# Kernel tuning notes

Measured on AMD Instinct MI355X. Metric: run time of the kernel, lower is better.

Reference implementation:

```python
import jax, jax.numpy as jnp
import numpy as np

B, L, DIN, W, H, NL = 4, 1024, 768, 12288, 8, 2
BOTTLENECK = 64
DB = W // BOTTLENECK        # 192: total bottlenecked attention dim
HD = DB // H                # 24: per-head dim
K = 32                      # topk
LAM = 1.0 / (4 * DIN)
EPS = 1e-6


def setup_inputs() -> dict:
    key = jax.random.key(0)
    ks = jax.random.split(key, 8)
    x_input = jax.random.normal(ks[0], (B, L, DIN), jnp.float32)
    # decoder dictionary (torch: randn; scaled for numeric stability)
    D = jax.random.normal(ks[1], (W, DIN), jnp.float32) * 0.02
    b = jnp.zeros((1, DIN), jnp.float32)
    # per-attn-layer bottlenecked projections, stacked over layers
    Wq = jax.random.normal(ks[2], (NL, W, DB), jnp.float32) * 0.02
    Wk = jax.random.normal(ks[3], (NL, W, DB), jnp.float32) * 0.02
    Wv = jax.random.normal(ks[4], (NL, W, DB), jnp.float32) * 0.02
    Wo = jax.random.normal(ks[5], (NL, DB, W), jnp.float32) * 0.02
    bq = jnp.zeros((NL, DB), jnp.float32)
    bk = jnp.zeros((NL, DB), jnp.float32)
    bv = jnp.zeros((NL, DB), jnp.float32)
    bo = jnp.zeros((NL, W), jnp.float32)
    return {"x_input": x_input, "D": D, "b": b, "Wq": Wq, "bq": bq,
            "Wk": Wk, "bk": bk, "Wv": Wv, "bv": bv, "Wo": Wo, "bo": bo}


def _attention(z_ctx, z_in, Wq, bq, Wk, bk, Wv, bv, Wo, bo):
    # queries from current codes, keys/values from shifted context codes
    q = (z_in @ Wq + bq).reshape(B, L, H, HD)
    k = (z_ctx @ Wk + bk).reshape(B, L, H, HD)
    v = (z_ctx @ Wv + bv).reshape(B, L, H, HD)
    scores = jnp.einsum('bqhd,bkhd->bhqk', q, k) / np.sqrt(HD).astype(np.float32)
    causal = jnp.tril(jnp.ones((L, L), bool))  # query t sees ctx positions <= t
    scores = jnp.where(causal, scores, jnp.float32(-1e30))
    a = jax.nn.softmax(scores, axis=-1)
    o = jnp.einsum('bhqk,bkhd->bqhd', a, v).reshape(B, L, DB)
    return o @ Wo + bo


def reference(x_input, D, b, Wq, bq, Wk, bk, Wv, bv, Wo, bo):
    E = D.T  # tied weights
    x = x_input - b
    z_pred = jnp.zeros((B, L, W), x.dtype)
    for i in range(NL):
        z_in = jax.nn.relu((x * LAM) @ E)                       # [B,L,W]
        z_ctx = jnp.concatenate([jnp.zeros_like(z_in[:, :1]), z_in[:, :-1]], axis=1)
        z_pred_ = jax.nn.relu(_attention(z_ctx, z_in, Wq[i], bq[i], Wk[i], bk[i],
                                         Wv[i], bv[i], Wo[i], bo[i]))
        Dz = z_pred_ @ D                                        # [B,L,DIN]
        Dz_norm = jnp.linalg.norm(Dz, axis=-1, keepdims=True) + EPS
        proj_scale = jnp.sum(Dz * x, axis=-1, keepdims=True) / (Dz_norm ** 2)
        z_pred = z_pred + z_pred_ * proj_scale
        x = x - proj_scale * Dz
    # topk sparsification of the novel codes
    z_novel = jax.nn.relu((x * LAM) @ E)
    zf = z_novel.reshape(-1, W)                                 # [B*L, W]
    _, idx = jax.lax.top_k(zf, K)
    mask = jnp.zeros_like(zf).at[jnp.arange(zf.shape[0])[:, None], idx].set(1.0)
    z_novel = (zf * mask).reshape(B, L, W)
    x_recons = (z_novel + z_pred) @ D + b
    return x_recons
```

## Files before the change

### kernel.cpp

```cpp
#include <hip/hip_runtime.h>
#include <hip/hip_bf16.h>

typedef __attribute__((ext_vector_type(4))) float f32x4;
typedef __attribute__((ext_vector_type(8))) short short8;
typedef __attribute__((ext_vector_type(8))) unsigned short ushort8;
typedef __attribute__((ext_vector_type(4))) unsigned short ushort4v;
typedef __attribute__((ext_vector_type(4))) unsigned int uint4v;

#define DEVFN __device__ __forceinline__

DEVFN float b2f(unsigned short u) { return __uint_as_float(((unsigned)u) << 16); }
DEVFN unsigned short f2b(float f) {
  __hip_bfloat16 h = __float2bfloat16(f);
  return __builtin_bit_cast(unsigned short, h);
}

DEVFN void load_lds16(const void* g, void* l) {
  __builtin_amdgcn_global_load_lds(
      (const __attribute__((address_space(1))) unsigned int*)g,
      (__attribute__((address_space(3))) unsigned int*)l, 16, 0, 0);
}


__global__ void fill_out_zero(float* o, int n) {
  int i = blockIdx.x * 256 + threadIdx.x;
  if (i < n) o[i] = 0.0f;
}

__global__ __launch_bounds__(256) void init_x(
    const float* __restrict__ xin, const float* __restrict__ bvec,
    float* __restrict__ x, unsigned short* __restrict__ xb) {
  size_t i = (size_t)blockIdx.x * 256 + threadIdx.x;
  int col = (int)(i % 768);
  float v = xin[i] - bvec[col];
  x[i] = v;
  xb[i] = f2b(v);
}

__global__ __launch_bounds__(256) void fill_bias(
    float* __restrict__ buf, const float* __restrict__ bias, int ld) {
  size_t i = (size_t)blockIdx.x * 256 + threadIdx.x;
  buf[i] = bias ? bias[(int)(i % ld)] : 0.0f;
}

__global__ __launch_bounds__(256) void conv_f2b(
    const float* __restrict__ in, unsigned short* __restrict__ out) {
  size_t i = ((size_t)blockIdx.x * 256 + threadIdx.x) * 4;
  f32x4 v = *(const f32x4*)(in + i);
  ushort4v w;
#pragma unroll
  for (int e = 0; e < 4; ++e) w[e] = f2b(v[e]);
  *(ushort4v*)(out + i) = w;
}

__global__ __launch_bounds__(256) void transpose_f2b(
    const float* __restrict__ in, unsigned short* __restrict__ out,
    int R, int C) {
  __shared__ float tile[32][33];
  int r0 = blockIdx.x * 32, c0 = blockIdx.y * 32;
  int tx = threadIdx.x & 31, ty = threadIdx.x >> 5;
#pragma unroll
  for (int i = 0; i < 4; ++i)
    tile[ty + i * 8][tx] = in[(size_t)(r0 + ty + i * 8) * C + c0 + tx];
  __syncthreads();
#pragma unroll
  for (int i = 0; i < 4; ++i)
    out[(size_t)(c0 + ty + i * 8) * R + r0 + tx] = f2b(tile[tx][ty + i * 8]);
}

template <int GX, int GY, int GZ, int RX, int RG>
DEVFN void rect_decode(int bid, int& x, int& y, int& z) {
  constexpr int NRG = (GY * GZ) / RG;
  const int xcd = bid & 7;
  const int rr = bid >> 3;
  const int rgx = xcd % NRG, rxx = xcd / NRG;
  const int gl = rr % RG;
  int xl = rr / RG;
  xl = (xl + rgx * (RX / NRG)) % RX;
  const int g = rgx * RG + gl;
  x = rxx * RX + xl;
  y = g % GY;
  z = g / GY;
}

template <typename CT, bool RELU, int SC, bool BIAS, bool SPLITK,
          int GX, int GY, int GZ, int RX, int RG>
__global__ __launch_bounds__(512, 2) void gemm_bt2(
    const unsigned short* __restrict__ A, const unsigned short* __restrict__ B,
    CT* __restrict__ C, const float* __restrict__ bias,
    int K, int ldc, float alpha) {
  __shared__ unsigned short sA[2][256 * 64];
  __shared__ unsigned short sB[2][256 * 64];
  const int tid = threadIdx.x;
  const int wave = tid >> 6, lane = tid & 63;
  int bx, by, bz;
  rect_decode<GX, GY, GZ, RX, RG>((int)blockIdx.x, bx, by, bz);
  const int row0 = bx * 256, col0 = by * 256;
  const unsigned short* Ab = A + (size_t)row0 * K;
  const unsigned short* Bb = B + (size_t)col0 * K;
  const int srow = lane >> 3;
  const int swc = ((lane & 7) ^ srow) * 8;
  const int wm = wave & 1, wn = wave >> 1;
  const int lr = lane & 15;
  const int hi = lane >> 4;
  const int l7 = lane & 7;
  const int ksw0 = (hi ^ l7) * 8;
  const int ksw1 = ((4 + hi) ^ l7) * 8;
  const int klen = SPLITK ? (K / GZ) : K;
  const int kbeg = SPLITK ? bz * klen : 0;
  const int nt = klen / 64;
  f32x4 acc[8][4] = {};
  auto stage = [&](int buf, int t) {
    const int k0 = kbeg + t * 64;
#pragma unroll
    for (int it = 0; it < 8; ++it) {
      int c = wave * 8 + it;
      if (c < 32) {
        int r = c * 8 + srow;
        load_lds16(Ab + (size_t)r * K + k0 + swc, &sA[buf][c * 512]);
      } else {
        int cb = c - 32;
        int r = cb * 8 + srow;
        load_lds16(Bb + (size_t)r * K + k0 + swc, &sB[buf][cb * 512]);
      }
    }
  };
  stage(0, 0);
  __syncthreads();
  for (int t = 0; t < nt; ++t) {
    const int cur = t & 1;
    if (t + 1 < nt) stage(cur ^ 1, t + 1);
    const unsigned short* cA = &sA[cur][0];
    const unsigned short* cB = &sB[cur][0];
#pragma unroll
    for (int ks = 0; ks < 2; ++ks) {
      const int ko = ks ? ksw1 : ksw0;
      short8 af[8], bfr[4];
#pragma unroll
      for (int i = 0; i < 8; ++i)
        af[i] = *(const short8*)&cA[(wm * 128 + i * 16 + lr) * 64 + ko];
#pragma unroll
      for (int j = 0; j < 4; ++j)
        bfr[j] = *(const short8*)&cB[(wn * 64 + j * 16 + lr) * 64 + ko];
#pragma unroll
      for (int i = 0; i < 8; ++i)
#pragma unroll
        for (int j = 0; j < 4; ++j)
          acc[i][j] = __builtin_amdgcn_mfma_f32_16x16x32_bf16(af[i], bfr[j], acc[i][j], 0, 0, 0);
    }
    __syncthreads();
  }
  const int rc = (SC == 0) ? 0 : ((row0 >> 10) + 1);
  const int rbase = row0 + rc + wm * 128 + (lane >> 4) * 4;
  const int cbase = col0 + wn * 64 + lr;
#pragma unroll
  for (int j = 0; j < 4; ++j) {
    int col = cbase + j * 16;
    float bv = BIAS ? bias[col] : 0.0f;
#pragma unroll
    for (int i = 0; i < 8; ++i) {
#pragma unroll
      for (int r = 0; r < 4; ++r) {
        float vv = acc[i][j][r] * alpha;
        size_t off = (size_t)(rbase + i * 16 + r) * ldc + col;
        if constexpr (SPLITK) {
          atomicAdd((float*)C + off, vv);
        } else {
          vv += bv;
          if (RELU) vv = fmaxf(vv, 0.0f);
          if constexpr (sizeof(CT) == 2) ((unsigned short*)C)[off] = f2b(vv);
          else C[off] = vv;
        }
      }
    }
  }
}

__global__ __launch_bounds__(256) void gemm_qkv(
    const unsigned short* __restrict__ A, const unsigned short* __restrict__ Bq,
    const float* __restrict__ bq, const float* __restrict__ bk,
    const float* __restrict__ bv,
    float* __restrict__ qb, float* __restrict__ kb, float* __restrict__ vb,
    float* __restrict__ P2) {
  __shared__ unsigned short sA[2][64 * 64];
  __shared__ unsigned short sB[2][192 * 64];
  const int tid = threadIdx.x;
  const int wave = tid >> 6, lane = tid & 63;
  const int bid = (int)blockIdx.x;
  const int xcd = bid & 7;
  const int rr = bid >> 3;
  const int grank = xcd * 48 + rr;
  const int combo = grank >> 6;
  const int row = grank & 63;
  const int wz = combo >> 1;
  const int s = combo & 1;
  const int shift = (wz > 0);
  const unsigned short* B = Bq + (size_t)wz * 192 * 12288;
  const float* bias = (wz == 0) ? bq : (wz == 1 ? bk : bv);
  float* dst = (s == 0) ? ((wz == 0) ? qb : (wz == 1 ? kb : vb))
                        : (P2 + (size_t)wz * 786432);
  const int row0 = row * 64;
  const int ra = (row0 >> 10) + 1;
  const unsigned short* Ab = A + (size_t)(row0 + ra) * 12288;
  const int srow = lane >> 3;
  const int swc = ((lane & 7) ^ srow) * 8;
  const int wm = wave & 1, wn = wave >> 1;
  const int lr = lane & 15;
  const int hi = lane >> 4;
  const int l7 = lane & 7;
  const int ksw0 = (hi ^ l7) * 8;
  const int ksw1 = ((4 + hi) ^ l7) * 8;
  const int kbeg = s * 6144;
  f32x4 acc[2][6] = {};
  auto stage = [&](int buf, int t) {
    const int k0 = kbeg + t * 64;
#pragma unroll
    for (int it = 0; it < 8; ++it) {
      int c = wave * 8 + it;
      if (c < 8) {
        int r = c * 8 + srow;
        load_lds16(Ab + (size_t)r * 12288 + k0 + swc, &sA[buf][c * 512]);
      } else {
        int cb = c - 8;
        int r = cb * 8 + srow;
        load_lds16(B + (size_t)r * 12288 + k0 + swc, &sB[buf][cb * 512]);
      }
    }
  };
  stage(0, 0);
  __syncthreads();
  for (int t = 0; t < 96; ++t) {
    const int cur = t & 1;
    if (t + 1 < 96) stage(cur ^ 1, t + 1);
    const unsigned short* cA = &sA[cur][0];
    const unsigned short* cB = &sB[cur][0];
#pragma unroll
    for (int ks = 0; ks < 2; ++ks) {
      const int ko = ks ? ksw1 : ksw0;
      short8 af[2], bfr[6];
#pragma unroll
      for (int i = 0; i < 2; ++i)
        af[i] = *(const short8*)&cA[(wm * 32 + i * 16 + lr) * 64 + ko];
#pragma unroll
      for (int j = 0; j < 6; ++j)
        bfr[j] = *(const short8*)&cB[(wn * 96 + j * 16 + lr) * 64 + ko];
#pragma unroll
      for (int i = 0; i < 2; ++i)
#pragma unroll
        for (int j = 0; j < 6; ++j)
          acc[i][j] = __builtin_amdgcn_mfma_f32_16x16x32_bf16(af[i], bfr[j], acc[i][j], 0, 0, 0);
    }
    __syncthreads();
  }
  const int rbase = row0 + wm * 32 + (lane >> 4) * 4;
  const int cbase = wn * 96 + lr;
#pragma unroll
  for (int j = 0; j < 6; ++j) {
    int col = cbase + j * 16;
    float bvv = (s == 0) ? bias[col] : 0.0f;
#pragma unroll
    for (int i = 0; i < 2; ++i)
#pragma unroll
      for (int r = 0; r < 4; ++r) {
        int rw = rbase + i * 16 + r;
        if (shift) {
          if ((rw & 1023) == 1023) continue;
          rw += 1;
        }
        dst[(size_t)rw * 192 + col] = acc[i][j][r] + bvv;
      }
  }
}

__global__ __launch_bounds__(256) void qkv_merge(
    const float* __restrict__ P2, float* __restrict__ qb,
    float* __restrict__ kb, float* __restrict__ vb) {
  size_t i = ((size_t)blockIdx.x * 256 + threadIdx.x) * 4;
  const int plane = (int)(i / 786432);
  const size_t o = i - (size_t)plane * 786432;
  float* dst = plane == 0 ? qb : (plane == 1 ? kb : vb);
  f32x4 a = *(const f32x4*)(P2 + i);
  f32x4 b = *(const f32x4*)(dst + o);
#pragma unroll
  for (int e = 0; e < 4; ++e) b[e] += a[e];
  *(f32x4*)(dst + o) = b;
}

__global__ __launch_bounds__(256) void attn_pass1(
    const float* __restrict__ q, const float* __restrict__ k,
    const float* __restrict__ v, float* __restrict__ P) {
  const int wave = threadIdx.x >> 6, lane = threadIdx.x & 63;
  const int xcd = (int)blockIdx.x & 7;
  const int task = xcd * 1152 + ((int)blockIdx.x >> 3) * 4 + wave;
  const int bh = task / 288, t = task % 288;
  const int b = bh >> 3, h = bh & 7;
  int g8 = 0;
  while (4 * (g8 + 1) * (g8 + 2) <= t) ++g8;
  const int r = t - 4 * g8 * (g8 + 1);
  const int qg = g8 * 8 + r / (g8 + 1);
  const int chunk = r % (g8 + 1);
  const int qi = lane & 15, ks = lane >> 4;
  const int qpos = qg * 16 + qi;
  const int n = b * 1024 + qpos;
  const float scale = 0.20412414523193154f;
  float qv[24];
  const float* qr = q + (size_t)n * 192 + h * 24;
#pragma unroll
  for (int d = 0; d < 24; ++d) qv[d] = qr[d] * scale;
  float m = -1e30f, l = 0.0f, ov[24] = {};
  const float* kbp = k + (size_t)b * 1024 * 192 + h * 24;
  const float* vbp = v + (size_t)b * 1024 * 192 + h * 24;
  const int kend = min(qpos, chunk * 128 + 127);
  for (int kp = chunk * 128 + ks; kp <= kend; kp += 4) {
    const f32x4* kr = (const f32x4*)(kbp + (size_t)kp * 192);
    float s0 = 0.0f, s1 = 0.0f, s2 = 0.0f;
#pragma unroll
    for (int j = 0; j < 2; ++j) {
      f32x4 k0 = kr[j * 3 + 0], k1 = kr[j * 3 + 1], k2 = kr[j * 3 + 2];
#pragma unroll
      for (int e = 0; e < 4; ++e) {
        s0 += qv[(j * 3 + 0) * 4 + e] * k0[e];
        s1 += qv[(j * 3 + 1) * 4 + e] * k1[e];
        s2 += qv[(j * 3 + 2) * 4 + e] * k2[e];
      }
    }
    float s = s0 + s1 + s2;
    float mn = fmaxf(m, s);
    float corr = __expf(m - mn);
    float p = __expf(s - mn);
    const f32x4* vr = (const f32x4*)(vbp + (size_t)kp * 192);
    l = l * corr + p;
#pragma unroll
    for (int j = 0; j < 6; ++j) {
      f32x4 vvv = vr[j];
#pragma unroll
      for (int e = 0; e < 4; ++e) ov[j * 4 + e] = ov[j * 4 + e] * corr + p * vvv[e];
    }
    m = mn;
  }
#pragma unroll
  for (int off = 16; off < 64; off <<= 1) {
    float m2 = __shfl_xor(m, off);
    float l2 = __shfl_xor(l, off);
    float mn = fmaxf(m, m2);
    float c1 = __expf(m - mn), c2 = __expf(m2 - mn);
    l = l * c1 + l2 * c2;
#pragma unroll
    for (int d = 0; d < 24; ++d) {
      float o2 = __shfl_xor(ov[d], off);
      ov[d] = ov[d] * c1 + o2 * c2;
    }
    m = mn;
  }
  if (ks == 0) {
    float* pr = P + ((size_t)task * 16 + qi) * 28;
    pr[0] = m;
    pr[1] = l;
#pragma unroll
    for (int d = 0; d < 24; ++d) pr[2 + d] = ov[d];
  }
}

__global__ __launch_bounds__(192) void attn_merge(
    const float* __restrict__ P, unsigned short* __restrict__ o) {
  const int n = blockIdx.x;
  const int tid = threadIdx.x;
  const int h = tid / 24, d = tid - h * 24;
  const int b = n >> 10, qpos = n & 1023;
  const int qg = qpos >> 4, qi = qpos & 15;
  const int g8 = qg >> 3;
  const int nch = g8 + 1;
  const int bh = b * 8 + h;
  const int base = bh * 288 + 4 * g8 * (g8 + 1) + (qg - g8 * 8) * (g8 + 1);
  float M = -1e30f;
  for (int c = 0; c < nch; ++c)
    M = fmaxf(M, P[((size_t)(base + c) * 16 + qi) * 28]);
  float L = 0.0f, OV = 0.0f;
  for (int c = 0; c < nch; ++c) {
    const float* pr = P + ((size_t)(base + c) * 16 + qi) * 28;
    float w = __expf(pr[0] - M);
    L += pr[1] * w;
    OV += pr[2 + d] * w;
  }
  o[(size_t)n * 192 + h * 24 + d] = f2b(OV / L);
}

__global__ __launch_bounds__(256) void proj_update(
    const float* __restrict__ Dz, float* __restrict__ x,
    unsigned short* __restrict__ xb) {
  const int n = blockIdx.x;
  const int tid = threadIdx.x;
  const float* dz = Dz + (size_t)n * 768;
  float* xr = x + (size_t)n * 768;
  float dot = 0.0f, s2 = 0.0f;
  for (int i = tid; i < 768; i += 256) {
    float a = dz[i], c = xr[i];
    dot += a * c;
    s2 += a * a;
  }
#pragma unroll
  for (int o2 = 32; o2; o2 >>= 1) {
    dot += __shfl_down(dot, o2);
    s2 += __shfl_down(s2, o2);
  }
  __shared__ float sd[4], ss[4], sp;
  const int wave = tid >> 6, lane = tid & 63;
  if (lane == 0) { sd[wave] = dot; ss[wave] = s2; }
  __syncthreads();
  if (tid == 0) {
    float Dd = sd[0] + sd[1] + sd[2] + sd[3];
    float S = ss[0] + ss[1] + ss[2] + ss[3];
    float nrm = sqrtf(S) + 1e-6f;
    sp = Dd / (nrm * nrm);
  }
  __syncthreads();
  float p = sp;
  for (int i = tid; i < 768; i += 256) {
    float nx = xr[i] - p * dz[i];
    xr[i] = nx;
    xb[(size_t)n * 768 + i] = f2b(nx);
  }
}

DEVFN int sanitize(int v) { return (v & 0x8000) ? 0 : v; }

__global__ __launch_bounds__(256) void topk_rows(
    const unsigned short* __restrict__ zbuf, int* __restrict__ idxo,
    float* __restrict__ valo) {
  const int n = blockIdx.x;
  const int b = n >> 10;
  const int tid = threadIdx.x;
  const int wave = tid >> 6, lane = tid & 63;
  const uint4v* zr = (const uint4v*)(zbuf + (size_t)(n + b + 1) * 12288);
  uint4v pk[6];
#pragma unroll
  for (int j = 0; j < 6; ++j) pk[j] = zr[tid * 6 + j];
  __shared__ int swsum[4];
  __shared__ int seq[256];
  __shared__ int spcnt;
  int lo = 0, hi = 0x7F7F;
  while (lo < hi) {
    int mid = (lo + hi) >> 1;
    int c = 0;
#pragma unroll
    for (int j = 0; j < 6; ++j)
#pragma unroll
      for (int e = 0; e < 4; ++e) {
        unsigned int u = pk[j][e];
        c += (sanitize((int)(u & 0xffffu)) > mid) + (sanitize((int)(u >> 16)) > mid);
      }
#pragma unroll
    for (int o2 = 32; o2; o2 >>= 1) c += __shfl_down(c, o2);
    if (lane == 0) swsum[wave] = c;
    __syncthreads();
    int total = swsum[0] + swsum[1] + swsum[2] + swsum[3];
    __syncthreads();
    if (total < 32) hi = mid; else lo = mid + 1;
  }
  const int T = lo;
  int cgt = 0, ceq = 0;
#pragma unroll
  for (int j = 0; j < 6; ++j)
#pragma unroll
    for (int e = 0; e < 4; ++e) {
      unsigned int u = pk[j][e];
      int v0 = sanitize((int)(u & 0xffffu)), v1 = sanitize((int)(u >> 16));
      cgt += (v0 > T) + (v1 > T);
      ceq += (v0 == T) + (v1 == T);
    }
  int cg = cgt;
#pragma unroll
  for (int o2 = 32; o2; o2 >>= 1) cg += __shfl_down(cg, o2);
  if (lane == 0) swsum[wave] = cg;
  seq[tid] = ceq;
  if (tid == 0) spcnt = 0;
  __syncthreads();
  const int total_gt = swsum[0] + swsum[1] + swsum[2] + swsum[3];
  for (int o2 = 1; o2 < 256; o2 <<= 1) {
    int vv = (tid >= o2) ? seq[tid - o2] : 0;
    __syncthreads();
    seq[tid] += vv;
    __syncthreads();
  }
  const int quota = 32 - total_gt;
  int rank = seq[tid] - ceq;
  int* irow = idxo + (size_t)n * 32;
  float* vrow = valo + (size_t)n * 32;
#pragma unroll
  for (int j = 0; j < 6; ++j)
#pragma unroll
    for (int e = 0; e < 4; ++e) {
      unsigned int u = pk[j][e];
#pragma unroll
      for (int hf = 0; hf < 2; ++hf) {
        int v = sanitize(hf ? (int)(u >> 16) : (int)(u & 0xffffu));
        bool kp = false;
        if (v > T) kp = true;
        else if (v == T) { if (rank < quota) kp = true; ++rank; }
        if (kp) {
          int pos = atomicAdd(&spcnt, 1);
          irow[pos] = tid * 48 + j * 8 + e * 2 + hf;
          vrow[pos] = b2f((unsigned short)v);
        }
      }
    }
}

__global__ __launch_bounds__(256) void sparse_recons(
    const int* __restrict__ idxo, const float* __restrict__ valo,
    const float* __restrict__ x, const float* __restrict__ xin,
    const float* __restrict__ D, float* __restrict__ out) {
  const int n = blockIdx.x;
  const int t = threadIdx.x;
  __shared__ int sidx[32];
  __shared__ float sval[32];
  if (t < 32) { sidx[t] = idxo[(size_t)n * 32 + t]; sval[t] = valo[(size_t)n * 32 + t]; }
  __syncthreads();
  float acc[3];
#pragma unroll
  for (int u = 0; u < 3; ++u) {
    size_t i = (size_t)n * 768 + t + u * 256;
    acc[u] = xin[i] - x[i];
  }
  for (int j = 0; j < 32; ++j) {
    size_t base = (size_t)sidx[j] * 768;
    float vj = sval[j];
#pragma unroll
    for (int u = 0; u < 3; ++u) acc[u] += vj * D[base + t + u * 256];
  }
#pragma unroll
  for (int u = 0; u < 3; ++u) out[(size_t)n * 768 + t + u * 256] = acc[u];
}

extern "C" void kernel_launch(void* const* d_in, const int* in_sizes, int n_in,
                              void* d_out, int out_size, void* d_ws, size_t ws_size,
                              hipStream_t stream) {
  (void)in_sizes; (void)n_in;
  const float* xin  = (const float*)d_in[0];
  const float* D    = (const float*)d_in[1];
  const float* bvec = (const float*)d_in[2];
  const float* Wq   = (const float*)d_in[3];
  const float* bq   = (const float*)d_in[4];
  const float* Wk   = (const float*)d_in[5];
  const float* bk   = (const float*)d_in[6];
  const float* Wv   = (const float*)d_in[7];
  const float* bv   = (const float*)d_in[8];
  const float* Wo   = (const float*)d_in[9];
  const float* bo   = (const float*)d_in[10];
  const float LAM = 1.0f / 3072.0f;

  char* ws = (char*)d_ws;
  size_t off = 0;
  auto alloc = [&](size_t bytes) {
    void* p = ws + off;
    off += (bytes + 255) & ~(size_t)255;
    return p;
  };
  unsigned short* zbuf = (unsigned short*)alloc((size_t)4 * 1025 * 12288 * 2);
  unsigned short* zpred_ = zbuf;
  float* attnP = (float*)zbuf;
  float* x           = (float*)alloc((size_t)4096 * 768 * 4);
  unsigned short* xb = (unsigned short*)alloc((size_t)4096 * 768 * 2);
  float* qb  = (float*)alloc((size_t)4096 * 192 * 4);
  float* kb  = (float*)alloc((size_t)4096 * 192 * 4);
  float* vb  = (float*)alloc((size_t)4096 * 192 * 4);
  unsigned short* ob = (unsigned short*)alloc((size_t)4096 * 192 * 2);
  float* Dz  = (float*)alloc((size_t)4096 * 768 * 4);
  int* idxo  = (int*)alloc((size_t)4096 * 32 * 4);
  float* valo = (float*)alloc((size_t)4096 * 32 * 4);
  const size_t WQKV = (size_t)192 * 12288;
  unsigned short* WqkvT = (unsigned short*)alloc((size_t)6 * WQKV * 2);
  unsigned short* WoT   = (unsigned short*)alloc((size_t)2 * 12288 * 192 * 2);
  unsigned short* Dbt   = (unsigned short*)alloc((size_t)12288 * 768 * 2);
  unsigned short* Dt    = (unsigned short*)alloc((size_t)768 * 12288 * 2);
  const size_t NEED = off;
  float* P2 = Dz;

  if (ws_size < NEED) {
    fill_out_zero<<<(out_size + 255) / 256, 256, 0, stream>>>((float*)d_out, out_size);
    return;
  }

  init_x<<<12288, 256, 0, stream>>>(xin, bvec, x, xb);
  conv_f2b<<<9216, 256, 0, stream>>>(D, Dbt);
  transpose_f2b<<<dim3(384, 24), 256, 0, stream>>>(D, Dt, 12288, 768);
  for (int l = 0; l < 2; ++l) {
    transpose_f2b<<<dim3(384, 6), 256, 0, stream>>>(
        Wq + (size_t)l * 12288 * 192, WqkvT + (size_t)(l * 3 + 0) * WQKV, 12288, 192);
    transpose_f2b<<<dim3(384, 6), 256, 0, stream>>>(
        Wk + (size_t)l * 12288 * 192, WqkvT + (size_t)(l * 3 + 1) * WQKV, 12288, 192);
    transpose_f2b<<<dim3(384, 6), 256, 0, stream>>>(
        Wv + (size_t)l * 12288 * 192, WqkvT + (size_t)(l * 3 + 2) * WQKV, 12288, 192);
    transpose_f2b<<<dim3(6, 384), 256, 0, stream>>>(
        Wo + (size_t)l * 192 * 12288, WoT + (size_t)l * 12288 * 192, 192, 12288);
  }

  for (int l = 0; l < 2; ++l) {
    gemm_bt2<unsigned short, true, 1, false, false, 16, 48, 1, 16, 6>
        <<<768, 512, 0, stream>>>(xb, Dbt, zbuf, nullptr, 768, 12288, LAM);
    fill_bias<<<3072, 256, 0, stream>>>(kb, bk + (size_t)l * 192, 192);
    fill_bias<<<3072, 256, 0, stream>>>(vb, bv + (size_t)l * 192, 192);
    fill_bias<<<9216, 256, 0, stream>>>(P2, nullptr, 192);
    gemm_qkv<<<384, 256, 0, stream>>>(
        zbuf, WqkvT + (size_t)(l * 3) * WQKV,
        bq + (size_t)l * 192, bk + (size_t)l * 192, bv + (size_t)l * 192,
        qb, kb, vb, P2);
    qkv_merge<<<2304, 256, 0, stream>>>(P2, qb, kb, vb);
    attn_pass1<<<2304, 256, 0, stream>>>(qb, kb, vb, attnP);
    attn_merge<<<4096, 192, 0, stream>>>(attnP, ob);
    gemm_bt2<unsigned short, true, 0, true, false, 16, 48, 1, 16, 6>
        <<<768, 512, 0, stream>>>(
        ob, WoT + (size_t)l * 12288 * 192, zpred_, bo + (size_t)l * 12288, 192, 12288, 1.0f);
    fill_bias<<<12288, 256, 0, stream>>>(Dz, nullptr, 768);
    gemm_bt2<float, false, 0, false, true, 16, 3, 4, 8, 3>
        <<<192, 512, 0, stream>>>(zpred_, Dt, Dz, nullptr, 12288, 768, 1.0f);
    proj_update<<<4096, 256, 0, stream>>>(Dz, x, xb);
  }
  gemm_bt2<unsigned short, true, 1, false, false, 16, 48, 1, 16, 6>
      <<<768, 512, 0, stream>>>(xb, Dbt, zbuf, nullptr, 768, 12288, LAM);
  topk_rows<<<4096, 256, 0, stream>>>(zbuf, idxo, valo);
  sparse_recons<<<4096, 256, 0, stream>>>(idxo, valo, x, xin, D, (float*)d_out);
}
```

Before: 1.419 ms.

## Stage K/V chunks in shared memory shared across four query-group waves

Attention pass1 now assigns one block per (batch-head, 64-query group, 128-key chunk). The block cooperatively loads the 128x24 K and V tiles into LDS, and all four waves (one per 16-query group) read them from there instead of each wave reading global memory. The task decomposition and the partial-result indexing in the merge kernel are reworked to match. The cost is an extra LDS footprint and a block-wide sync. Waves covering early queries may also idle on diagonal chunks.

```diff
diff --git a/kernel.cpp b/kernel.cpp
--- a/kernel.cpp
+++ b/kernel.cpp
@@ -289,30 +289,54 @@
 __global__ __launch_bounds__(256) void attn_pass1(
     const float* __restrict__ q, const float* __restrict__ k,
     const float* __restrict__ v, float* __restrict__ P) {
-  const int wave = threadIdx.x >> 6, lane = threadIdx.x & 63;
+  __shared__ float sK[128 * 24];
+  __shared__ float sV[128 * 24];
+  const int tid = threadIdx.x;
+  const int wave = tid >> 6, lane = tid & 63;
   const int xcd = (int)blockIdx.x & 7;
-  const int task = xcd * 1152 + ((int)blockIdx.x >> 3) * 4 + wave;
-  const int bh = task / 288, t = task % 288;
+  const int r0 = (int)blockIdx.x >> 3;
+  const int bh = xcd * 4 + r0 / 72;
+  const int t = r0 % 72;
   const int b = bh >> 3, h = bh & 7;
-  int g8 = 0;
-  while (4 * (g8 + 1) * (g8 + 2) <= t) ++g8;
-  const int r = t - 4 * g8 * (g8 + 1);
-  const int qg = g8 * 8 + r / (g8 + 1);
-  const int chunk = r % (g8 + 1);
+  int jq = 0;
+  while (true) {
+    int jn = jq + 1;
+    int a2 = jn >> 1;
+    int offn = a2 * a2 + a2 + (jn & 1) * (a2 + 1);
+    if (jn < 16 && offn <= t) jq = jn; else break;
+  }
+  const int aq = jq >> 1;
+  const int offj = aq * aq + aq + (jq & 1) * (aq + 1);
+  const int c = t - offj;
+  const int qg = jq * 4 + wave;
   const int qi = lane & 15, ks = lane >> 4;
   const int qpos = qg * 16 + qi;
   const int n = b * 1024 + qpos;
+  const int task = bh * 72 + t;
+  {
+    const float* kg = k + (size_t)(b * 1024 + c * 128) * 192 + h * 24;
+    const float* vg = v + (size_t)(b * 1024 + c * 128) * 192 + h * 24;
+#pragma unroll
+    for (int i = 0; i < 3; ++i) {
+      int idx = tid + i * 256;
+      int row = idx / 6, seg = idx - row * 6;
+      *(f32x4*)&sK[row * 24 + seg * 4] =
+          *(const f32x4*)(kg + (size_t)row * 192 + seg * 4);
+      *(f32x4*)&sV[row * 24 + seg * 4] =
+          *(const f32x4*)(vg + (size_t)row * 192 + seg * 4);
+    }
+  }
   const float scale = 0.20412414523193154f;
   float qv[24];
   const float* qr = q + (size_t)n * 192 + h * 24;
 #pragma unroll
   for (int d = 0; d < 24; ++d) qv[d] = qr[d] * scale;
+  __syncthreads();
   float m = -1e30f, l = 0.0f, ov[24] = {};
-  const float* kbp = k + (size_t)b * 1024 * 192 + h * 24;
-  const float* vbp = v + (size_t)b * 1024 * 192 + h * 24;
-  const int kend = min(qpos, chunk * 128 + 127);
-  for (int kp = chunk * 128 + ks; kp <= kend; kp += 4) {
-    const f32x4* kr = (const f32x4*)(kbp + (size_t)kp * 192);
+  const int kb0 = c * 128;
+  const int kend = min(qpos, kb0 + 127);
+  for (int kp = kb0 + ks; kp <= kend; kp += 4) {
+    const f32x4* kr = (const f32x4*)&sK[(kp - kb0) * 24];
     float s0 = 0.0f, s1 = 0.0f, s2 = 0.0f;
 #pragma unroll
     for (int j = 0; j < 2; ++j) {
@@ -328,7 +352,7 @@
     float mn = fmaxf(m, s);
     float corr = __expf(m - mn);
     float p = __expf(s - mn);
-    const f32x4* vr = (const f32x4*)(vbp + (size_t)kp * 192);
+    const f32x4* vr = (const f32x4*)&sV[(kp - kb0) * 24];
     l = l * corr + p;
 #pragma unroll
     for (int j = 0; j < 6; ++j) {
@@ -353,7 +377,7 @@
     m = mn;
   }
   if (ks == 0) {
-    float* pr = P + ((size_t)task * 16 + qi) * 28;
+    float* pr = P + ((size_t)task * 64 + wave * 16 + qi) * 28;
     pr[0] = m;
     pr[1] = l;
 #pragma unroll
@@ -368,19 +392,21 @@
   const int h = tid / 24, d = tid - h * 24;
   const int b = n >> 10, qpos = n & 1023;
   const int qg = qpos >> 4, qi = qpos & 15;
-  const int g8 = qg >> 3;
-  const int nch = g8 + 1;
+  const int j = qg >> 2, w = qg & 3;
+  const int a = j >> 1;
+  const int nch = a + 1;
+  const int offj = a * a + a + (j & 1) * (a + 1);
   const int bh = b * 8 + h;
-  const int base = bh * 288 + 4 * g8 * (g8 + 1) + (qg - g8 * 8) * (g8 + 1);
+  const int base = bh * 72 + offj;
   float M = -1e30f;
-  for (int c = 0; c < nch; ++c)
-    M = fmaxf(M, P[((size_t)(base + c) * 16 + qi) * 28]);
+  for (int cc = 0; cc < nch; ++cc)
+    M = fmaxf(M, P[((size_t)(base + cc) * 64 + w * 16 + qi) * 28]);
   float L = 0.0f, OV = 0.0f;
-  for (int c = 0; c < nch; ++c) {
-    const float* pr = P + ((size_t)(base + c) * 16 + qi) * 28;
-    float w = __expf(pr[0] - M);
-    L += pr[1] * w;
-    OV += pr[2 + d] * w;
+  for (int cc = 0; cc < nch; ++cc) {
+    const float* pr = P + ((size_t)(base + cc) * 64 + w * 16 + qi) * 28;
+    float wgt = __expf(pr[0] - M);
+    L += pr[1] * wgt;
+    OV += pr[2 + d] * wgt;
   }
   o[(size_t)n * 192 + h * 24 + d] = f2b(OV / L);
 }
```

Result: faster. 1.309 ms (-7.8%).
